# Performance work log

Hardware: AMD Instinct MI355X
Metric: run time of the kernel (lower is better)

## Reference

```python
import jax, jax.numpy as jnp
import numpy as np

LN_EPS = 1e-5
NUM_HEADS = 16

def _layernorm(x, g, b):
    mu = jnp.mean(x, axis=-1, keepdims=True)
    var = jnp.mean(jnp.square(x - mu), axis=-1, keepdims=True)
    return (x - mu) * jax.lax.rsqrt(var + LN_EPS) * g + b

def setup_inputs() -> dict:
    key = jax.random.key(0)
    ks = jax.random.split(key, 8)
    B, N, C, Hf = 8, 4096, 1024, 2048
    s = 1.0 / np.sqrt(C)
    return {
        "x": jax.random.normal(ks[0], (B, N, C), jnp.float32),
        "ln1_g": jnp.ones((C,), jnp.float32),
        "ln1_b": jnp.zeros((C,), jnp.float32),
        "ln2_g": jnp.ones((C,), jnp.float32),
        "ln2_b": jnp.zeros((C,), jnp.float32),
        "wq": jax.random.normal(ks[1], (C, C), jnp.float32) * s,
        "wk": jax.random.normal(ks[2], (C, C), jnp.float32) * s,
        "wv": jax.random.normal(ks[3], (C, C), jnp.float32) * s,
        "proj_w": jax.random.normal(ks[4], (C, C), jnp.float32) * s,
        "proj_b": jnp.zeros((C,), jnp.float32),
        "fc1_w": jax.random.normal(ks[5], (C, Hf), jnp.float32) * s,
        "fc1_b": jnp.zeros((Hf,), jnp.float32),
        "fc2_w": jax.random.normal(ks[6], (Hf, C), jnp.float32) / np.sqrt(Hf),
        "fc2_b": jnp.zeros((C,), jnp.float32),
    }

def reference(x, ln1_g, ln1_b, ln2_g, ln2_b, wq, wk, wv, proj_w, proj_b,
              fc1_w, fc1_b, fc2_w, fc2_b):
    B, N, C = x.shape
    H = NUM_HEADS
    d = C // H
    scale = d ** -0.5

    # --- attention branch (note: attention over the head_dim axis, d x d scores) ---
    h = _layernorm(x, ln1_g, ln1_b)
    def split(t):  # (B,N,C) -> (B,H,d,N), matching permute(0,2,3,1)
        return jnp.transpose(t.reshape(B, N, H, d), (0, 2, 3, 1))
    q = split(h @ wq)
    k = split(h @ wk)
    v = split(h @ wv)
    attn = jax.nn.softmax(jnp.einsum("bhdn,bhen->bhde", q, k) * scale, axis=-1)  # (B,H,d,d)
    o = jnp.einsum("bhde,bhen->bhdn", attn, v)           # (B,H,d,N)
    o = jnp.transpose(o, (0, 2, 1, 3)).reshape(B, N, C)  # transpose(1,2).reshape
    x = x + (o @ proj_w + proj_b)

    # --- MLP branch ---
    h2 = _layernorm(x, ln2_g, ln2_b)
    h2 = jax.nn.gelu(h2 @ fc1_w + fc1_b, approximate=False)
    x = x + (h2 @ fc2_w + fc2_b)
    return x
```

## Files before the change

kernel.cpp:

```cpp
#include <hip/hip_runtime.h>
#include <cmath>

typedef __attribute__((ext_vector_type(8))) _Float16 f16x8;
typedef __attribute__((ext_vector_type(8))) unsigned short u16x8;
typedef __attribute__((ext_vector_type(4))) float f32x4;

__device__ __forceinline__ unsigned short f2h(float f) {
  return __builtin_bit_cast(unsigned short, (_Float16)f);
}
__device__ __forceinline__ float h2f(unsigned short u) {
  return (float)__builtin_bit_cast(_Float16, u);
}

__device__ __forceinline__ void async16(const void* gp, void* lp) {
  __builtin_amdgcn_global_load_lds(
      (const __attribute__((address_space(1))) void*)gp,
      (__attribute__((address_space(3))) void*)lp, 16, 0, 0);
}

struct TCArgs {
  const float* W[6];
  unsigned short* T[6];
  int K[6];
  int N[6];
};

__global__ __launch_bounds__(256) void transpose_cast6(TCArgs a) {
  const int z = blockIdx.z;
  const int K = a.K[z], N = a.N[z];
  const int n0 = blockIdx.x * 32, k0 = blockIdx.y * 32;
  if (n0 >= N || k0 >= K) return;
  const float* __restrict__ W = a.W[z];
  unsigned short* __restrict__ WT = a.T[z];
  __shared__ float tile[32][33];
  const int tx = threadIdx.x & 31, ty = threadIdx.x >> 5;
#pragma unroll
  for (int r = 0; r < 4; ++r)
    tile[ty + 8 * r][tx] = W[(size_t)(k0 + ty + 8 * r) * N + n0 + tx];
  __syncthreads();
#pragma unroll
  for (int r = 0; r < 4; ++r)
    WT[(size_t)(n0 + ty + 8 * r) * K + k0 + tx] = f2h(tile[tx][ty + 8 * r]);
}

__global__ __launch_bounds__(256) void layernorm_cast(
    const float* __restrict__ x, const float* __restrict__ g,
    const float* __restrict__ bt, unsigned short* __restrict__ out) {
  const int row = blockIdx.x, tid = threadIdx.x;
  const float4 v = ((const float4*)(x + (size_t)row * 1024))[tid];
  float s = v.x + v.y + v.z + v.w;
  float ss = v.x * v.x + v.y * v.y + v.z * v.z + v.w * v.w;
#pragma unroll
  for (int off = 32; off >= 1; off >>= 1) {
    s += __shfl_down(s, off);
    ss += __shfl_down(ss, off);
  }
  __shared__ float red[10];
  const int wave = tid >> 6, lane = tid & 63;
  if (lane == 0) { red[wave] = s; red[4 + wave] = ss; }
  __syncthreads();
  if (tid == 0) {
    float S = red[0] + red[1] + red[2] + red[3];
    float SS = red[4] + red[5] + red[6] + red[7];
    float mu = S * (1.f / 1024.f);
    float var = SS * (1.f / 1024.f) - mu * mu;
    red[8] = mu;
    red[9] = rsqrtf(var + 1e-5f);
  }
  __syncthreads();
  const float mu = red[8], rs = red[9];
  const float4 gv = ((const float4*)g)[tid];
  const float4 bv = ((const float4*)bt)[tid];
  ushort4 r;
  r.x = f2h((v.x - mu) * rs * gv.x + bv.x);
  r.y = f2h((v.y - mu) * rs * gv.y + bv.y);
  r.z = f2h((v.z - mu) * rs * gv.z + bv.z);
  r.w = f2h((v.w - mu) * rs * gv.w + bv.w);
  ((ushort4*)(out + (size_t)row * 1024))[tid] = r;
}

__global__ __launch_bounds__(256) void resid_ln(
    const float* __restrict__ x, const unsigned short* __restrict__ pr,
    const float* __restrict__ pb, const float* __restrict__ g,
    const float* __restrict__ bt, float* __restrict__ out,
    unsigned short* __restrict__ h2) {
  const int row = blockIdx.x, tid = threadIdx.x;
  const size_t off = (size_t)row * 1024;
  const float4 xv = ((const float4*)(x + off))[tid];
  const ushort4 pv = ((const ushort4*)(pr + off))[tid];
  const float4 bb = ((const float4*)pb)[tid];
  float4 v;
  v.x = xv.x + h2f(pv.x) + bb.x;
  v.y = xv.y + h2f(pv.y) + bb.y;
  v.z = xv.z + h2f(pv.z) + bb.z;
  v.w = xv.w + h2f(pv.w) + bb.w;
  ((float4*)(out + off))[tid] = v;
  float s = v.x + v.y + v.z + v.w;
  float ss = v.x * v.x + v.y * v.y + v.z * v.z + v.w * v.w;
#pragma unroll
  for (int o = 32; o >= 1; o >>= 1) {
    s += __shfl_down(s, o);
    ss += __shfl_down(ss, o);
  }
  __shared__ float red[10];
  const int wave = tid >> 6, lane = tid & 63;
  if (lane == 0) { red[wave] = s; red[4 + wave] = ss; }
  __syncthreads();
  if (tid == 0) {
    float S = red[0] + red[1] + red[2] + red[3];
    float SS = red[4] + red[5] + red[6] + red[7];
    float mu = S * (1.f / 1024.f);
    float var = SS * (1.f / 1024.f) - mu * mu;
    red[8] = mu;
    red[9] = rsqrtf(var + 1e-5f);
  }
  __syncthreads();
  const float mu = red[8], rs = red[9];
  const float4 gv = ((const float4*)g)[tid];
  const float4 bv = ((const float4*)bt)[tid];
  ushort4 r;
  r.x = f2h((v.x - mu) * rs * gv.x + bv.x);
  r.y = f2h((v.y - mu) * rs * gv.y + bv.y);
  r.z = f2h((v.z - mu) * rs * gv.z + bv.z);
  r.w = f2h((v.w - mu) * rs * gv.w + bv.w);
  ((ushort4*)(h2 + off))[tid] = r;
}


#define STAGE_A(TT, KKH)                                                       \
  {                                                                            \
    unsigned short* d = smem + ((TT) & 1) * 32768 + (KKH) * 8192 + wave * 512; \
    const unsigned short* sp_ = pA + (size_t)(TT) * 64 + (KKH) * 32;           \
    async16(sp_, d);                                                           \
    async16(sp_ + rstep, d + 4096);                                            \
  }

#define STAGE_B(TT, KKH)                                                       \
  {                                                                            \
    unsigned short* d =                                                        \
        smem + ((TT) & 1) * 32768 + 16384 + (KKH) * 8192 + wave * 512;         \
    const unsigned short* sp_ = pB + (size_t)(TT) * 64 + (KKH) * 32;           \
    async16(sp_, d);                                                           \
    async16(sp_ + rstep, d + 4096);                                            \
  }

#define GPHASE(KK, MH, STAGE, TAILW)                                           \
  {                                                                            \
    f16x8 af[4];                                                               \
    _Pragma("unroll") for (int i = 0; i < 4; ++i) {                            \
      const int ra = wm * 128 + ((MH)*4 + i) * 16 + l16;                       \
      af[i] = __builtin_bit_cast(                                              \
          f16x8, *(const u16x8*)&bufA[(KK)*8192 + ra * 32 +                    \
                                      ((g16 ^ ((ra >> 1) & 3)) * 8)]);         \
    }                                                                          \
    if ((MH) == 0) {                                                           \
      _Pragma("unroll") for (int j = 0; j < 4; ++j) {                          \
        const int rb = wn * 64 + j * 16 + l16;                                 \
        bf[j] = __builtin_bit_cast(                                            \
            f16x8, *(const u16x8*)&bufB[(KK)*8192 + rb * 32 +                  \
                                        ((g16 ^ ((rb >> 1) & 3)) * 8)]);       \
      }                                                                        \
    }                                                                          \
    __builtin_amdgcn_sched_barrier(0);                                         \
    STAGE;                                                                     \
    __builtin_amdgcn_sched_barrier(0);                                         \
    __builtin_amdgcn_s_barrier();                                              \
    asm volatile("s_waitcnt lgkmcnt(0)" ::: "memory");                         \
    __builtin_amdgcn_sched_barrier(0);                                         \
    __builtin_amdgcn_s_setprio(1);                                             \
    _Pragma("unroll") for (int i = 0; i < 4; ++i)                              \
        _Pragma("unroll") for (int j = 0; j < 4; ++j) acc[(MH)*4 + i][j] =     \
        __builtin_amdgcn_mfma_f32_16x16x32_f16(af[i], bf[j],                   \
                                               acc[(MH)*4 + i][j], 0, 0, 0);   \
    __builtin_amdgcn_s_setprio(0);                                             \
    __builtin_amdgcn_sched_barrier(0);                                         \
    TAILW;                                                                     \
    __builtin_amdgcn_s_barrier();                                              \
  }

__global__ __launch_bounds__(512) void gemm256(
    const unsigned short* __restrict__ A, const unsigned short* __restrict__ BT,
    int M, int N, int K,
    const float* __restrict__ bias, unsigned short* __restrict__ outB, int gelu,
    float* __restrict__ resid, const float* __restrict__ rbias) {
  __shared__ __align__(16) unsigned short smem[65536];
  const int tid = threadIdx.x, wave = tid >> 6, lane = tid & 63;
  const int l16 = lane & 15, g16 = lane >> 4;
  const int wm = wave >> 2, wn = wave & 3;

  const int lin = blockIdx.y * gridDim.x + blockIdx.x;
  const int t_ = lin >> 3;
  const int bx = t_ % gridDim.x;
  const int by = (lin & 7) + 8 * (t_ / gridDim.x);
  const int row0 = by * 256, col0 = bx * 256;

  const int r_ = tid >> 2;
  const int s_ = ((tid & 3) ^ ((tid >> 3) & 3)) * 8;
  const unsigned short* pA = A + (size_t)(row0 + r_) * K + s_;
  const unsigned short* pB = BT + (size_t)(col0 + r_) * K + s_;
  const size_t rstep = (size_t)128 * K;
  const int NT = K >> 6;

  f32x4 acc[8][4] = {};

  STAGE_B(0, 0);
  STAGE_A(0, 0);
  STAGE_B(0, 1);
  STAGE_A(0, 1);
  STAGE_B(1, 0);
  STAGE_A(1, 0);
  STAGE_B(1, 1);
  __builtin_amdgcn_sched_barrier(0);
  asm volatile("s_waitcnt vmcnt(6)" ::: "memory");
  __builtin_amdgcn_s_barrier();

  for (int t = 0; t < NT - 2; ++t) {
    const unsigned short* bufA = smem + (t & 1) * 32768;
    const unsigned short* bufB = bufA + 16384;
    f16x8 bf[4];
    GPHASE(0, 0, STAGE_A(t + 1, 1), )
    GPHASE(0, 1, STAGE_B(t + 2, 0), )
    GPHASE(1, 0, STAGE_A(t + 2, 0), )
    GPHASE(1, 1, STAGE_B(t + 2, 1),
           asm volatile("s_waitcnt vmcnt(6)" ::: "memory"))
  }

  {
    const int t = NT - 2;
    const unsigned short* bufA = smem + (t & 1) * 32768;
    const unsigned short* bufB = bufA + 16384;
    f16x8 bf[4];
    GPHASE(0, 0, STAGE_A(t + 1, 1), )
    GPHASE(0, 1, , )
    GPHASE(1, 0, , )
    GPHASE(1, 1, , asm volatile("s_waitcnt vmcnt(0)" ::: "memory"))
  }
  {
    const int t = NT - 1;
    const unsigned short* bufA = smem + (t & 1) * 32768;
    const unsigned short* bufB = bufA + 16384;
    f16x8 bf[4];
    GPHASE(0, 0, , )
    GPHASE(0, 1, , )
    GPHASE(1, 0, , )
    GPHASE(1, 1, , )
  }

  unsigned short* scr = smem + wave * 4352;
#pragma unroll
  for (int mh = 0; mh < 2; ++mh) {
#pragma unroll
    for (int j = 0; j < 4; ++j) {
      const float bcol = gelu ? bias[col0 + wn * 64 + j * 16 + l16] : 0.f;
#pragma unroll
      for (int i = 0; i < 4; ++i)
#pragma unroll
        for (int r = 0; r < 4; ++r) {
          float val = acc[mh * 4 + i][j][r] + bcol;
          if (gelu) val = 0.5f * val * (1.0f + erff(val * 0.70710678118f));
          scr[(i * 16 + g16 * 4 + r) * 68 + j * 16 + l16] = f2h(val);
        }
    }
    if (resid) {
#pragma unroll
      for (int rr = 0; rr < 8; ++rr) {
        const int lr = rr * 8 + (lane >> 3);
        const int lc = (lane & 7) * 8;
        const u16x8 val = *(const u16x8*)&scr[lr * 68 + lc];
        const int grow = row0 + wm * 128 + mh * 64 + lr;
        const int gcol = col0 + wn * 64 + lc;
        float* po = resid + (size_t)grow * N + gcol;
        const float4 b0 = ((const float4*)(rbias + gcol))[0];
        const float4 b1 = ((const float4*)(rbias + gcol))[1];
        float4 o0 = ((const float4*)po)[0];
        float4 o1 = ((const float4*)po)[1];
        o0.x += h2f(val[0]) + b0.x;
        o0.y += h2f(val[1]) + b0.y;
        o0.z += h2f(val[2]) + b0.z;
        o0.w += h2f(val[3]) + b0.w;
        o1.x += h2f(val[4]) + b1.x;
        o1.y += h2f(val[5]) + b1.y;
        o1.z += h2f(val[6]) + b1.z;
        o1.w += h2f(val[7]) + b1.w;
        ((float4*)po)[0] = o0;
        ((float4*)po)[1] = o1;
      }
    } else {
#pragma unroll
      for (int rr = 0; rr < 8; ++rr) {
        const int lr = rr * 8 + (lane >> 3);
        const int lc = (lane & 7) * 8;
        const u16x8 val = *(const u16x8*)&scr[lr * 68 + lc];
        *(u16x8*)(outB + (size_t)(row0 + wm * 128 + mh * 64 + lr) * N + col0 +
                  wn * 64 + lc) = val;
      }
    }
  }
}

__global__ __launch_bounds__(256) void attn_qk_part(
    const unsigned short* __restrict__ qkv, float* __restrict__ sp) {
  constexpr int ST = 72;
  __shared__ unsigned short sQT[64 * ST];
  __shared__ unsigned short sKT[64 * ST];
  const int bx = blockIdx.x, bh = bx >> 2, chunk = bx & 3;
  const int b = bh >> 4, h = bh & 15;
  const size_t base = (size_t)b * 4096 * 3072 + (size_t)h * 64;
  const int tid = threadIdx.x, wave = tid >> 6, lane = tid & 63;
  const int l16 = lane & 15, g16 = lane >> 4;
  const int wm = wave & 1, wn = wave >> 1;
  const int srow = tid >> 2, sseg = tid & 3;

  f32x4 acc[2][2] = {};

  for (int ntl = 0; ntl < 16; ++ntl) {
    const int nt = chunk * 16 + ntl;
    __syncthreads();
    const size_t roff = base + (size_t)(nt * 64 + srow) * 3072 + sseg * 16;
    const u16x8 q0 = *(const u16x8*)(qkv + roff);
    const u16x8 q1 = *(const u16x8*)(qkv + roff + 8);
    const u16x8 k0 = *(const u16x8*)(qkv + roff + 1024);
    const u16x8 k1 = *(const u16x8*)(qkv + roff + 1032);
#pragma unroll
    for (int ii = 0; ii < 8; ++ii) {
      sQT[(sseg * 16 + ii) * ST + srow] = q0[ii];
      sQT[(sseg * 16 + 8 + ii) * ST + srow] = q1[ii];
      sKT[(sseg * 16 + ii) * ST + srow] = k0[ii];
      sKT[(sseg * 16 + 8 + ii) * ST + srow] = k1[ii];
    }
    __syncthreads();
#pragma unroll
    for (int kk = 0; kk < 2; ++kk) {
      f16x8 aq[2], bk[2];
#pragma unroll
      for (int i = 0; i < 2; ++i)
        aq[i] = __builtin_bit_cast(f16x8,
            *(const u16x8*)&sQT[(wm * 32 + i * 16 + l16) * ST + kk * 32 + g16 * 8]);
#pragma unroll
      for (int j = 0; j < 2; ++j)
        bk[j] = __builtin_bit_cast(f16x8,
            *(const u16x8*)&sKT[(wn * 32 + j * 16 + l16) * ST + kk * 32 + g16 * 8]);
#pragma unroll
      for (int i = 0; i < 2; ++i)
#pragma unroll
        for (int j = 0; j < 2; ++j)
          acc[i][j] = __builtin_amdgcn_mfma_f32_16x16x32_f16(aq[i], bk[j], acc[i][j], 0, 0, 0);
    }
  }

  float* o = sp + (size_t)bx * 4096;
#pragma unroll
  for (int i = 0; i < 2; ++i)
#pragma unroll
    for (int j = 0; j < 2; ++j)
#pragma unroll
      for (int r = 0; r < 4; ++r)
        o[(wm * 32 + i * 16 + g16 * 4 + r) * 64 + (wn * 32 + j * 16 + l16)] = acc[i][j][r];
}

__global__ __launch_bounds__(256) void attn_softmax(
    const float* __restrict__ sp, unsigned short* __restrict__ am) {
  const int gid = blockIdx.x * 4 + (threadIdx.x >> 6);
  const int lane = threadIdx.x & 63;
  const int bh = gid >> 6, dd = gid & 63;
  const float* p = sp + (size_t)bh * 16384 + dd * 64 + lane;
  const float v = p[0] + p[4096] + p[8192] + p[12288];
  float mx = v;
#pragma unroll
  for (int o = 32; o >= 1; o >>= 1) mx = fmaxf(mx, __shfl_xor(mx, o));
  const float e = __expf(0.125f * (v - mx));
  float s = e;
#pragma unroll
  for (int o = 32; o >= 1; o >>= 1) s += __shfl_xor(s, o);
  am[(size_t)bh * 4096 + dd * 64 + lane] = f2h(e / s);
}

__global__ __launch_bounds__(256) void attn_pv(
    const unsigned short* __restrict__ qkv, const unsigned short* __restrict__ am,
    unsigned short* __restrict__ o) {
  __shared__ unsigned short pvs[4 * 1088];
  const int bx = blockIdx.x, bh = bx >> 2, chunk = bx & 3;
  const int b = bh >> 4, h = bh & 15;
  const size_t base = (size_t)b * 4096 * 3072 + (size_t)h * 64;
  const int tid = threadIdx.x, wave = tid >> 6, lane = tid & 63;
  const int l16 = lane & 15, g16 = lane >> 4;
  const int wm = wave & 1, wn = wave >> 1;
  unsigned short* tw = pvs + wave * 1088;

  f16x8 amf[2][2];
#pragma unroll
  for (int i = 0; i < 2; ++i)
#pragma unroll
    for (int kk = 0; kk < 2; ++kk)
      amf[i][kk] = __builtin_bit_cast(f16x8,
          *(const u16x8*)(am + (size_t)bh * 4096 +
                          (wm * 32 + i * 16 + l16) * 64 + kk * 32 + g16 * 8));

  for (int ntl = 0; ntl < 16; ++ntl) {
    const int nt = chunk * 16 + ntl;
    f32x4 oc[2][2] = {};
#pragma unroll
    for (int kk = 0; kk < 2; ++kk) {
#pragma unroll
      for (int j = 0; j < 2; ++j) {
        const f16x8 vf = __builtin_bit_cast(f16x8,
            *(const u16x8*)(qkv + base + 2048 +
                            (size_t)(nt * 64 + wn * 32 + j * 16 + l16) * 3072 +
                            kk * 32 + g16 * 8));
#pragma unroll
        for (int i = 0; i < 2; ++i)
          oc[i][j] = __builtin_amdgcn_mfma_f32_16x16x32_f16(amf[i][kk], vf, oc[i][j], 0, 0, 0);
      }
    }
    asm volatile("s_waitcnt lgkmcnt(0)" ::: "memory");
#pragma unroll
    for (int i = 0; i < 2; ++i)
#pragma unroll
      for (int j = 0; j < 2; ++j)
#pragma unroll
        for (int r = 0; r < 4; ++r)
          tw[(i * 16 + g16 * 4 + r) * 34 + j * 16 + l16] = f2h(oc[i][j][r]);
    asm volatile("s_waitcnt lgkmcnt(0)" ::: "memory");
    const int rt = lane >> 1;
    const int c0 = (lane & 1) * 16;
#pragma unroll
    for (int c2 = 0; c2 < 2; ++c2) {
      const int ct = c0 + c2 * 8;
      const u16x8 v8 = *(const u16x8*)&tw[rt * 34 + ct];
      const int row = b * 4096 + (wm * 32 + rt) * 64 + h * 4 + chunk;
      *(u16x8*)(o + (size_t)row * 1024 + ntl * 64 + wn * 32 + ct) = v8;
    }
  }
}

extern "C" void kernel_launch(void* const* d_in, const int* in_sizes, int n_in,
                              void* d_out, int out_size, void* d_ws, size_t ws_size,
                              hipStream_t stream) {
  (void)in_sizes; (void)n_in; (void)out_size; (void)ws_size;
  const float* x = (const float*)d_in[0];
  const float* ln1g = (const float*)d_in[1];
  const float* ln1b = (const float*)d_in[2];
  const float* ln2g = (const float*)d_in[3];
  const float* ln2b = (const float*)d_in[4];
  const float* wq = (const float*)d_in[5];
  const float* wk = (const float*)d_in[6];
  const float* wv = (const float*)d_in[7];
  const float* projw = (const float*)d_in[8];
  const float* projb = (const float*)d_in[9];
  const float* fc1w = (const float*)d_in[10];
  const float* fc1b = (const float*)d_in[11];
  const float* fc2w = (const float*)d_in[12];
  const float* fc2b = (const float*)d_in[13];
  float* out = (float*)d_out;

  const int M = 8 * 4096, C = 1024, HF = 2048;
  const size_t MC = (size_t)M * C;

  unsigned short* p = (unsigned short*)d_ws;
  unsigned short* wqkvT = p; p += (size_t)3 * C * C;
  unsigned short* prT = p; p += (size_t)C * C;
  unsigned short* f1T = p; p += (size_t)HF * C;
  unsigned short* f2T = p; p += (size_t)C * HF;
  unsigned short* hb = p;  p += MC;
  unsigned short* qkvb = p; p += 3 * MC;
  float* Spart = (float*)hb;
  unsigned short* Am = wqkvT;
  unsigned short* ob = hb;
  unsigned short* projout = qkvb;
  unsigned short* h2 = qkvb + 2 * MC;
  unsigned short* h3 = qkvb;
  unsigned short* yb = hb;

  TCArgs ta;
  ta.W[0] = wq;    ta.T[0] = wqkvT;                     ta.K[0] = C;  ta.N[0] = C;
  ta.W[1] = wk;    ta.T[1] = wqkvT + (size_t)C * C;     ta.K[1] = C;  ta.N[1] = C;
  ta.W[2] = wv;    ta.T[2] = wqkvT + (size_t)2 * C * C; ta.K[2] = C;  ta.N[2] = C;
  ta.W[3] = projw; ta.T[3] = prT;                       ta.K[3] = C;  ta.N[3] = C;
  ta.W[4] = fc1w;  ta.T[4] = f1T;                       ta.K[4] = C;  ta.N[4] = HF;
  ta.W[5] = fc2w;  ta.T[5] = f2T;                       ta.K[5] = HF; ta.N[5] = C;
  transpose_cast6<<<dim3(HF / 32, HF / 32, 6), 256, 0, stream>>>(ta);

  layernorm_cast<<<M, 256, 0, stream>>>(x, ln1g, ln1b, hb);

  gemm256<<<dim3(3 * C / 256, M / 256), 512, 0, stream>>>(
      hb, wqkvT, M, 3 * C, C, nullptr, qkvb, 0, nullptr, nullptr);

  attn_qk_part<<<512, 256, 0, stream>>>(qkvb, Spart);
  attn_softmax<<<2048, 256, 0, stream>>>(Spart, Am);
  attn_pv<<<512, 256, 0, stream>>>(qkvb, Am, ob);

  gemm256<<<dim3(C / 256, M / 256), 512, 0, stream>>>(
      ob, prT, M, C, C, nullptr, projout, 0, nullptr, nullptr);

  resid_ln<<<M, 256, 0, stream>>>(x, projout, projb, ln2g, ln2b, out, h2);

  gemm256<<<dim3(HF / 256, M / 256), 512, 0, stream>>>(
      h2, f1T, M, HF, C, fc1b, h3, 1, nullptr, nullptr);

  gemm256<<<dim3(C / 256, M / 256), 512, 0, stream>>>(
      h3, f2T, M, C, HF, nullptr, yb, 0, out, fc2b);
}
```

Measured before the change: 1.096 ms.

## Fuse attention softmax into PV kernel and drop a GEMM mainloop barrier

Removes the standalone softmax kernel: each attn_pv block now sums the four partial QK score slices, computes the row softmax in registers with shuffle reductions, and stores the normalized fp16 matrix in shared memory before the PV MFMAs. This saves one launch and a global round trip for the attention matrix, though the softmax is now recomputed by each of the four chunk blocks per head. It also deletes one s_barrier between staging and compute in the GEMM macro, which could create an LDS race if the remaining barrier does not cover it. Scratch buffers are reassigned, with the attention output staged in the output buffer.

```diff
diff --git a/kernel.cpp b/kernel.cpp
--- a/kernel.cpp
+++ b/kernel.cpp
@@ -164,7 +164,6 @@
     __builtin_amdgcn_sched_barrier(0);                                         \
     STAGE;                                                                     \
     __builtin_amdgcn_sched_barrier(0);                                         \
-    __builtin_amdgcn_s_barrier();                                              \
     asm volatile("s_waitcnt lgkmcnt(0)" ::: "memory");                         \
     __builtin_amdgcn_sched_barrier(0);                                         \
     __builtin_amdgcn_s_setprio(1);                                             \
@@ -358,26 +357,10 @@
         o[(wm * 32 + i * 16 + g16 * 4 + r) * 64 + (wn * 32 + j * 16 + l16)] = acc[i][j][r];
 }
 
-__global__ __launch_bounds__(256) void attn_softmax(
-    const float* __restrict__ sp, unsigned short* __restrict__ am) {
-  const int gid = blockIdx.x * 4 + (threadIdx.x >> 6);
-  const int lane = threadIdx.x & 63;
-  const int bh = gid >> 6, dd = gid & 63;
-  const float* p = sp + (size_t)bh * 16384 + dd * 64 + lane;
-  const float v = p[0] + p[4096] + p[8192] + p[12288];
-  float mx = v;
-#pragma unroll
-  for (int o = 32; o >= 1; o >>= 1) mx = fmaxf(mx, __shfl_xor(mx, o));
-  const float e = __expf(0.125f * (v - mx));
-  float s = e;
-#pragma unroll
-  for (int o = 32; o >= 1; o >>= 1) s += __shfl_xor(s, o);
-  am[(size_t)bh * 4096 + dd * 64 + lane] = f2h(e / s);
-}
-
 __global__ __launch_bounds__(256) void attn_pv(
-    const unsigned short* __restrict__ qkv, const unsigned short* __restrict__ am,
+    const unsigned short* __restrict__ qkv, const float* __restrict__ sp,
     unsigned short* __restrict__ o) {
+  __shared__ unsigned short amL[64 * 68];
   __shared__ unsigned short pvs[4 * 1088];
   const int bx = blockIdx.x, bh = bx >> 2, chunk = bx & 3;
   const int b = bh >> 4, h = bh & 15;
@@ -387,14 +370,39 @@
   const int wm = wave & 1, wn = wave >> 1;
   unsigned short* tw = pvs + wave * 1088;
 
+  {
+    const int r = tid >> 2, q = tid & 3;
+    const float* p0 = sp + (size_t)bh * 16384 + r * 64 + q * 16;
+    float v[16];
+#pragma unroll
+    for (int j = 0; j < 16; ++j)
+      v[j] = p0[j] + p0[4096 + j] + p0[8192 + j] + p0[12288 + j];
+    float mx = v[0];
+#pragma unroll
+    for (int j = 1; j < 16; ++j) mx = fmaxf(mx, v[j]);
+    mx = fmaxf(mx, __shfl_xor(mx, 1));
+    mx = fmaxf(mx, __shfl_xor(mx, 2));
+    float s = 0.f;
+#pragma unroll
+    for (int j = 0; j < 16; ++j) {
+      v[j] = __expf(0.125f * (v[j] - mx));
+      s += v[j];
+    }
+    s += __shfl_xor(s, 1);
+    s += __shfl_xor(s, 2);
+    const float inv = 1.0f / s;
+#pragma unroll
+    for (int j = 0; j < 16; ++j) amL[r * 68 + q * 16 + j] = f2h(v[j] * inv);
+  }
+  __syncthreads();
+
   f16x8 amf[2][2];
 #pragma unroll
   for (int i = 0; i < 2; ++i)
 #pragma unroll
     for (int kk = 0; kk < 2; ++kk)
       amf[i][kk] = __builtin_bit_cast(f16x8,
-          *(const u16x8*)(am + (size_t)bh * 4096 +
-                          (wm * 32 + i * 16 + l16) * 64 + kk * 32 + g16 * 8));
+          *(const u16x8*)&amL[(wm * 32 + i * 16 + l16) * 68 + kk * 32 + g16 * 8]);
 
   for (int ntl = 0; ntl < 16; ++ntl) {
     const int nt = chunk * 16 + ntl;
@@ -464,12 +472,10 @@
   unsigned short* hb = p;  p += MC;
   unsigned short* qkvb = p; p += 3 * MC;
   float* Spart = (float*)hb;
-  unsigned short* Am = wqkvT;
-  unsigned short* ob = hb;
+  unsigned short* ob = (unsigned short*)out;
   unsigned short* projout = qkvb;
   unsigned short* h2 = qkvb + 2 * MC;
   unsigned short* h3 = qkvb;
-  unsigned short* yb = hb;
 
   TCArgs ta;
   ta.W[0] = wq;    ta.T[0] = wqkvT;                     ta.K[0] = C;  ta.N[0] = C;
@@ -486,8 +492,7 @@
       hb, wqkvT, M, 3 * C, C, nullptr, qkvb, 0, nullptr, nullptr);
 
   attn_qk_part<<<512, 256, 0, stream>>>(qkvb, Spart);
-  attn_softmax<<<2048, 256, 0, stream>>>(Spart, Am);
-  attn_pv<<<512, 256, 0, stream>>>(qkvb, Am, ob);
+  attn_pv<<<512, 256, 0, stream>>>(qkvb, Spart, ob);
 
   gemm256<<<dim3(C / 256, M / 256), 512, 0, stream>>>(
       ob, prT, M, C, C, nullptr, projout, 0, nullptr, nullptr);
@@ -498,5 +503,5 @@
       h2, f1T, M, HF, C, fc1b, h3, 1, nullptr, nullptr);
 
   gemm256<<<dim3(C / 256, M / 256), 512, 0, stream>>>(
-      h3, f2T, M, C, HF, nullptr, yb, 0, out, fc2b);
-}
+      h3, f2T, M, C, HF, nullptr, qkvb, 0, out, fc2b);
+}
```

After: 1.120 ms. +2.2%, slower.
